# Performance work log

Hardware: AMD Instinct MI355X
Metric: run time of the kernel (lower is better)

## Reference

```python
import jax, jax.numpy as jnp
import numpy as np

B, N, T, D, H = 64, 207, 24, 128, 8
DK = D // H
EPS = 1e-5


def setup_inputs() -> dict:
    key = jax.random.key(0)
    ks = jax.random.split(key, 18)
    s = 1.0 / np.sqrt(D)
    inp = {
        "hidden": jax.random.normal(ks[0], (B, N, T, D), jnp.float32),
        "matrix": jax.random.uniform(ks[1], (B, T, N, N), jnp.float32) / N,
        "Wq": jax.random.normal(ks[2], (D, D), jnp.float32) * s,
        "bq": jnp.zeros((D,), jnp.float32),
        "Wk": jax.random.normal(ks[3], (D, D), jnp.float32) * s,
        "bk": jnp.zeros((D,), jnp.float32),
        "Wv": jax.random.normal(ks[4], (D, D), jnp.float32) * s,
        "bv": jnp.zeros((D,), jnp.float32),
        "Wo": jax.random.normal(ks[5], (D, D), jnp.float32) * s,
        "bo": jnp.zeros((D,), jnp.float32),
        "Wgcn": jax.random.normal(ks[6], (D, D), jnp.float32) * s,
        "bgcn": jnp.zeros((D,), jnp.float32),
        "Wgate": jax.random.normal(ks[7], (D, 2 * D), jnp.float32) * (1.0 / np.sqrt(2 * D)),
        "bgate": jnp.zeros((D,), jnp.float32),
        "gamma": jnp.ones((D,), jnp.float32),
        "beta": jnp.zeros((D,), jnp.float32),
    }
    return inp


def reference(hidden, matrix, Wq, bq, Wk, bk, Wv, bv, Wo, bo,
              Wgcn, bgcn, Wgate, bgate, gamma, beta):
    # ---- GCN branch: per-timestep A·X then channel mixing (dmodel->dmodel)
    # hidden: [B,N,T,D], matrix: [B,T,N,N] -> aggregated [B,N,T,D]
    agg = jnp.einsum('bntc,btnm->bmtc', hidden, matrix)
    gcn_out = agg @ Wgcn.T + bgcn                       # [B,N,T,D]

    # ---- Causal multi-head temporal attention
    q = (hidden @ Wq.T + bq).reshape(B, N, T, H, DK)
    k = (hidden @ Wk.T + bk).reshape(B, N, T, H, DK)
    v = (hidden @ Wv.T + bv).reshape(B, N, T, H, DK)
    scale = 1.0 / np.sqrt(DK)
    scores = jnp.einsum('bnthe,bnshe->bnhts', q, k)     # [B,N,H,T,T]
    causal = jnp.triu(jnp.ones((T, T), bool), k=1)      # mask future
    scores = jnp.where(causal, -jnp.inf, scores)
    attn = jax.nn.softmax(scale * scores, axis=-1)
    ctx = jnp.einsum('bnhts,bnshd->bnthd', attn, v).reshape(B, N, T, D)
    attn_out = ctx @ Wo.T + bo                          # [B,N,T,D]

    # ---- Gated fusion: concat -> linear -> batchnorm (training stats) -> sigmoid
    gate_in = jnp.concatenate([gcn_out, attn_out], axis=-1)  # [B,N,T,2D]
    g = gate_in @ Wgate.T + bgate                            # [B,N,T,D]
    mean = jnp.mean(g, axis=(0, 1, 2))
    var = jnp.var(g, axis=(0, 1, 2))
    g = (g - mean) * jax.lax.rsqrt(var + EPS) * gamma + beta
    z = jax.nn.sigmoid(g)
    return z * gcn_out + (1.0 - z) * attn_out
```

## Files before the change

kernel.cpp:

```cpp
#include <hip/hip_runtime.h>

#define B_ 64
#define N_ 207
#define T_ 24
#define D_ 128
#define H_ 8
#define MROWS (B_*N_*T_)
#define SELEMS ((size_t)MROWS * D_)
#define NBLK_FB 768
#define BNROWS_FB 414
#define NBLK_FUSED (MROWS/128)
#define EPS_ 1e-5f

typedef __attribute__((ext_vector_type(8))) short s16x8;
typedef __attribute__((ext_vector_type(4))) float f32x4;

#define MFMA16(a,b,c) __builtin_amdgcn_mfma_f32_16x16x32_bf16(a,b,c,0,0,0)

__device__ __forceinline__ float bfu2f(unsigned short u) {
  return __uint_as_float(((unsigned int)u) << 16);
}
__device__ __forceinline__ unsigned short f2bfu(float f) {
  unsigned int x = __float_as_uint(f);
  return (unsigned short)((x + 0x7fffu + ((x >> 16) & 1u)) >> 16);
}
__device__ __forceinline__ unsigned int packbf2(float lo, float hi) {
  return (unsigned int)f2bfu(lo) | ((unsigned int)f2bfu(hi) << 16);
}

__device__ __forceinline__ s16x8 fragA_from_f32(const float* __restrict__ p) {
  const float4 a = *(const float4*)p;
  const float4 b = *(const float4*)(p + 4);
  s16x8 r;
  r[0] = (short)f2bfu(a.x); r[1] = (short)f2bfu(a.y);
  r[2] = (short)f2bfu(a.z); r[3] = (short)f2bfu(a.w);
  r[4] = (short)f2bfu(b.x); r[5] = (short)f2bfu(b.y);
  r[6] = (short)f2bfu(b.z); r[7] = (short)f2bfu(b.w);
  return r;
}

__device__ __forceinline__ void epi_store_bf16(
    const f32x4 acc[2][8], const float* __restrict__ bias,
    unsigned short* __restrict__ Obase, unsigned short* __restrict__ lb, int l)
{
  const int lr = l & 15, lg = l >> 4;
  #pragma unroll
  for (int nt = 0; nt < 8; nt++) {
    const float b = bias[nt*16 + lr];
    #pragma unroll
    for (int mt = 0; mt < 2; mt++)
      #pragma unroll
      for (int r = 0; r < 4; r++)
        lb[(mt*16 + lg*4 + r)*136 + nt*16 + lr] = f2bfu(acc[mt][nt][r] + b);
  }
  #pragma unroll
  for (int p = 0; p < 8; p++) {
    const int c = p*64 + l;
    const int row = c >> 4, c8 = (c & 15) * 8;
    const s16x8 v = *(const s16x8*)&lb[row*136 + c8];
    *(s16x8*)(Obase + (size_t)row*D_ + c8) = v;
  }
}

__global__ __launch_bounds__(256) void k_wcast(
    const float* __restrict__ Wq, const float* __restrict__ Wk,
    const float* __restrict__ Wv, const float* __restrict__ Wo,
    const float* __restrict__ Wgcn, const float* __restrict__ Wgate,
    unsigned short* __restrict__ out)
{
  const int idx4 = (blockIdx.x * 256 + threadIdx.x) * 4;
  if (idx4 >= 114688) return;
  const float* src; int off;
  if      (idx4 < 16384) { src = Wq;    off = idx4; }
  else if (idx4 < 32768) { src = Wk;    off = idx4 - 16384; }
  else if (idx4 < 49152) { src = Wv;    off = idx4 - 32768; }
  else if (idx4 < 65536) { src = Wo;    off = idx4 - 49152; }
  else if (idx4 < 81920) { src = Wgcn;  off = idx4 - 65536; }
  else                   { src = Wgate; off = idx4 - 81920; }
  const float4 v = *(const float4*)(src + off);
  ushort4 u;
  u.x = f2bfu(v.x); u.y = f2bfu(v.y); u.z = f2bfu(v.z); u.w = f2bfu(v.w);
  *(ushort4*)(out + idx4) = u;
}

__global__ __launch_bounds__(256) void k_gcn2(
    const float* __restrict__ hidden, const float* __restrict__ matrix,
    const unsigned short* __restrict__ Wgcnb, const float* __restrict__ bgcn,
    unsigned short* __restrict__ gcn)
{
  __shared__ __align__(16) unsigned char smem[34816];
  unsigned short* Ms16 = (unsigned short*)smem;
  unsigned int*   Ms32 = (unsigned int*)smem;
  unsigned short* Hs16 = (unsigned short*)(smem + 10240);
  unsigned int*   Hs32 = (unsigned int*)(smem + 10240);
  unsigned short* GsAll = (unsigned short*)smem;

  const int tid = threadIdx.x;
  const int w = tid >> 6, l = tid & 63;
  const int lr = l & 15, lg = l >> 4;
  const int m0 = blockIdx.x * 128;
  const int by = (int)blockIdx.y;
  const int b = by / T_, t = by % T_;

  const int nn = (tid & 15) * 2;
  const int cb = (tid >> 4) * 8;

  const float* mbase = matrix + (size_t)(b*T_ + t)*N_*N_;
  const float* hbase = hidden + (size_t)b*N_*T_*D_ + (size_t)t*D_;

  f32x4 acc1[2][8];
  #pragma unroll
  for (int mt = 0; mt < 2; mt++)
    #pragma unroll
    for (int nt = 0; nt < 8; nt++)
      #pragma unroll
      for (int e = 0; e < 4; e++) acc1[mt][nt][e] = 0.f;

  for (int ch = 0; ch < 7; ++ch) {
    const int n0 = ch * 32;
    const int n_r0 = n0 + nn, n_r1 = n_r0 + 1;
    const bool rv0 = (n_r0 < N_), rv1 = (n_r1 < N_);
    const size_t nc0 = (size_t)(rv0 ? n_r0 : 0);
    const size_t nc1 = (size_t)(rv1 ? n_r1 : 0);

    float va[8], vb[8];
    {
      const float* r0 = mbase + nc0*N_ + m0 + cb;
      const float* r1 = mbase + nc1*N_ + m0 + cb;
      #pragma unroll
      for (int j = 0; j < 2; ++j) {
        const int mg = m0 + cb + j*4;
        if (mg + 3 < N_) {
          const float4 x0 = *(const float4*)(r0 + j*4);
          const float4 x1 = *(const float4*)(r1 + j*4);
          va[j*4+0]=x0.x; va[j*4+1]=x0.y; va[j*4+2]=x0.z; va[j*4+3]=x0.w;
          vb[j*4+0]=x1.x; vb[j*4+1]=x1.y; vb[j*4+2]=x1.z; vb[j*4+3]=x1.w;
        } else {
          #pragma unroll
          for (int e = 0; e < 4; ++e) {
            const bool ok = (mg + e) < N_;
            va[j*4+e] = ok ? r0[j*4+e] : 0.f;
            vb[j*4+e] = ok ? r1[j*4+e] : 0.f;
          }
        }
      }
      #pragma unroll
      for (int e = 0; e < 8; ++e) {
        if (!rv0) va[e] = 0.f;
        if (!rv1) vb[e] = 0.f;
      }
    }
    float ha[8], hb[8];
    {
      const float* r0 = hbase + nc0*(T_*D_) + cb;
      const float* r1 = hbase + nc1*(T_*D_) + cb;
      const float4 x0a = *(const float4*)(r0);
      const float4 x0b = *(const float4*)(r0 + 4);
      const float4 x1a = *(const float4*)(r1);
      const float4 x1b = *(const float4*)(r1 + 4);
      ha[0]=x0a.x; ha[1]=x0a.y; ha[2]=x0a.z; ha[3]=x0a.w;
      ha[4]=x0b.x; ha[5]=x0b.y; ha[6]=x0b.z; ha[7]=x0b.w;
      hb[0]=x1a.x; hb[1]=x1a.y; hb[2]=x1a.z; hb[3]=x1a.w;
      hb[4]=x1b.x; hb[5]=x1b.y; hb[6]=x1b.z; hb[7]=x1b.w;
      #pragma unroll
      for (int e = 0; e < 8; ++e) {
        if (!rv0) ha[e] = 0.f;
        if (!rv1) hb[e] = 0.f;
      }
    }
    __syncthreads();
    #pragma unroll
    for (int e = 0; e < 8; ++e)
      Ms32[(cb + e)*20 + (tid & 15)] = packbf2(va[e], vb[e]);
    #pragma unroll
    for (int e = 0; e < 8; ++e)
      Hs32[(cb + e)*20 + (tid & 15)] = packbf2(ha[e], hb[e]);
    __syncthreads();
    s16x8 af0 = *(const s16x8*)(Ms16 + (size_t)(w*32 +  0 + lr)*40 + lg*8);
    s16x8 af1 = *(const s16x8*)(Ms16 + (size_t)(w*32 + 16 + lr)*40 + lg*8);
    #pragma unroll
    for (int nt = 0; nt < 8; ++nt) {
      const s16x8 bf = *(const s16x8*)(Hs16 + (size_t)(nt*16 + lr)*40 + lg*8);
      acc1[0][nt] = MFMA16(af0, bf, acc1[0][nt]);
      acc1[1][nt] = MFMA16(af1, bf, acc1[1][nt]);
    }
  }

  __syncthreads();
  unsigned short* gs = GsAll + (size_t)w * (32*136);
  #pragma unroll
  for (int nt = 0; nt < 8; nt++)
    #pragma unroll
    for (int mt = 0; mt < 2; mt++)
      #pragma unroll
      for (int r = 0; r < 4; r++)
        gs[(mt*16 + lg*4 + r)*136 + nt*16 + lr] = f2bfu(acc1[mt][nt][r]);

  f32x4 acc2[2][8];
  #pragma unroll
  for (int mt = 0; mt < 2; mt++)
    #pragma unroll
    for (int nt = 0; nt < 8; nt++)
      #pragma unroll
      for (int e = 0; e < 4; e++) acc2[mt][nt][e] = 0.f;

  #pragma unroll
  for (int ks = 0; ks < 4; ++ks) {
    const s16x8 a0 = *(const s16x8*)(gs + (size_t)( 0 + lr)*136 + ks*32 + lg*8);
    const s16x8 a1 = *(const s16x8*)(gs + (size_t)(16 + lr)*136 + ks*32 + lg*8);
    #pragma unroll
    for (int nt = 0; nt < 8; ++nt) {
      const s16x8 bf = *(const s16x8*)(Wgcnb + (size_t)(nt*16 + lr)*D_ + ks*32 + lg*8);
      acc2[0][nt] = MFMA16(a0, bf, acc2[0][nt]);
      acc2[1][nt] = MFMA16(a1, bf, acc2[1][nt]);
    }
  }

  #pragma unroll
  for (int nt = 0; nt < 8; nt++) {
    const float bsc = bgcn[nt*16 + lr];
    #pragma unroll
    for (int mt = 0; mt < 2; mt++)
      #pragma unroll
      for (int r = 0; r < 4; r++)
        gs[(mt*16 + lg*4 + r)*136 + nt*16 + lr] = f2bfu(acc2[mt][nt][r] + bsc);
  }
  const size_t Obase = ((size_t)b*N_ + (m0 + w*32))*(size_t)(T_*D_) + (size_t)t*D_;
  #pragma unroll
  for (int p = 0; p < 8; p++) {
    const int c = p*64 + l;
    const int row = c >> 4, c8 = (c & 15) * 8;
    const int gm = m0 + w*32 + row;
    if (gm < N_) {
      const s16x8 v = *(const s16x8*)(gs + row*136 + c8);
      *(s16x8*)(gcn + Obase + (size_t)row*(T_*D_) + c8) = v;
    }
  }
}

__global__ __launch_bounds__(256) void k_qkv(
    const float* __restrict__ hidden,
    const unsigned short* __restrict__ Wqb, const unsigned short* __restrict__ Wkb,
    const unsigned short* __restrict__ Wvb,
    const float* __restrict__ bq, const float* __restrict__ bk,
    const float* __restrict__ bv,
    unsigned short* __restrict__ Q, unsigned short* __restrict__ K,
    unsigned short* __restrict__ V)
{
  __shared__ __align__(16) unsigned short lbuf[4][32*136];
  const int tid = threadIdx.x;
  const int w = tid >> 6, l = tid & 63;
  const int lr = l & 15, lg = l >> 4;
  const size_t m0 = (size_t)blockIdx.x * 128 + w * 32;

  s16x8 afr[2][4];
  #pragma unroll
  for (int mt = 0; mt < 2; mt++)
    #pragma unroll
    for (int ks = 0; ks < 4; ks++)
      afr[mt][ks] = fragA_from_f32(hidden + (m0 + mt*16 + lr)*D_ + ks*32 + lg*8);

  const unsigned short* Ws[3] = {Wqb, Wkb, Wvb};
  const float*          bs[3] = {bq, bk, bv};
  unsigned short*       Os[3] = {Q, K, V};
  #pragma unroll
  for (int out = 0; out < 3; out++) {
    const unsigned short* W = Ws[out];
    f32x4 acc[2][8];
    #pragma unroll
    for (int mt = 0; mt < 2; mt++)
      #pragma unroll
      for (int nt = 0; nt < 8; nt++)
        #pragma unroll
        for (int e = 0; e < 4; e++) acc[mt][nt][e] = 0.f;
    #pragma unroll
    for (int ks = 0; ks < 4; ks++) {
      #pragma unroll
      for (int nt = 0; nt < 8; nt++) {
        const s16x8 bf = *(const s16x8*)(W + (size_t)(nt*16 + lr)*D_ + ks*32 + lg*8);
        acc[0][nt] = MFMA16(afr[0][ks], bf, acc[0][nt]);
        acc[1][nt] = MFMA16(afr[1][ks], bf, acc[1][nt]);
      }
    }
    epi_store_bf16(acc, bs[out], Os[out] + m0*D_, lbuf[w], l);
  }
}

__global__ __launch_bounds__(256) void k_projWo(
    const unsigned short* __restrict__ A0,
    const unsigned short* __restrict__ Wb, const float* __restrict__ bias,
    unsigned short* __restrict__ OutP)
{
  __shared__ __align__(16) unsigned short lbuf[4][32*136];
  const int tid = threadIdx.x;
  const int w = tid >> 6, l = tid & 63;
  const int lr = l & 15, lg = l >> 4;
  const size_t m0 = (size_t)blockIdx.x * 128 + w * 32;

  f32x4 acc[2][8];
  #pragma unroll
  for (int mt = 0; mt < 2; mt++)
    #pragma unroll
    for (int nt = 0; nt < 8; nt++)
      #pragma unroll
      for (int e = 0; e < 4; e++) acc[mt][nt][e] = 0.f;

  #pragma unroll
  for (int ks = 0; ks < 4; ks++) {
    const s16x8 a0 = *(const s16x8*)(A0 + (m0 +  0 + lr)*D_ + ks*32 + lg*8);
    const s16x8 a1 = *(const s16x8*)(A0 + (m0 + 16 + lr)*D_ + ks*32 + lg*8);
    #pragma unroll
    for (int nt = 0; nt < 8; nt++) {
      const s16x8 bf = *(const s16x8*)(Wb + (size_t)(nt*16 + lr)*D_ + ks*32 + lg*8);
      acc[0][nt] = MFMA16(a0, bf, acc[0][nt]);
      acc[1][nt] = MFMA16(a1, bf, acc[1][nt]);
    }
  }
  epi_store_bf16(acc, bias, OutP + m0*D_, lbuf[w], l);
}

template<bool STATS>
__global__ __launch_bounds__(256) void k_gate(
    const unsigned short* __restrict__ A0, const unsigned short* __restrict__ A1,
    const unsigned short* __restrict__ Wb, const float* __restrict__ bias,
    float* __restrict__ Out, float* __restrict__ psum, float* __restrict__ psq)
{
  __shared__ float lbs[4*128], lbq[4*128];
  const int tid = threadIdx.x;
  const int w = tid >> 6, l = tid & 63;
  const int lr = l & 15, lg = l >> 4;
  const size_t m0 = (size_t)blockIdx.x * 128 + w * 32;

  f32x4 acc[2][8];
  #pragma unroll
  for (int mt = 0; mt < 2; mt++)
    #pragma unroll
    for (int nt = 0; nt < 8; nt++)
      #pragma unroll
      for (int e = 0; e < 4; e++) acc[mt][nt][e] = 0.f;

  #pragma unroll
  for (int ks = 0; ks < 8; ks++) {
    const unsigned short* Asrc = (ks >= 4) ? A1 : A0;
    const int kk = (ks >= 4) ? ks - 4 : ks;
    const s16x8 a0 = *(const s16x8*)(Asrc + (m0 +  0 + lr)*D_ + kk*32 + lg*8);
    const s16x8 a1 = *(const s16x8*)(Asrc + (m0 + 16 + lr)*D_ + kk*32 + lg*8);
    #pragma unroll
    for (int nt = 0; nt < 8; nt++) {
      const s16x8 bf = *(const s16x8*)(Wb + (size_t)(nt*16 + lr)*256 + ks*32 + lg*8);
      acc[0][nt] = MFMA16(a0, bf, acc[0][nt]);
      acc[1][nt] = MFMA16(a1, bf, acc[1][nt]);
    }
  }

  #pragma unroll
  for (int nt = 0; nt < 8; nt++) {
    const float b = bias[nt*16 + lr];
    float s = 0.f, q = 0.f;
    #pragma unroll
    for (int mt = 0; mt < 2; mt++)
      #pragma unroll
      for (int r = 0; r < 4; r++) {
        const float v = acc[mt][nt][r] + b;
        Out[(m0 + mt*16 + lg*4 + r)*D_ + nt*16 + lr] = v;
        if (STATS) { s += v; q += v*v; }
      }
    if (STATS) {
      s += __shfl_xor(s, 16); s += __shfl_xor(s, 32);
      q += __shfl_xor(q, 16); q += __shfl_xor(q, 32);
      if (lg == 0) {
        lbs[w*128 + nt*16 + lr] = s;
        lbq[w*128 + nt*16 + lr] = q;
      }
    }
  }
  if (STATS) {
    __syncthreads();
    if (tid < 128) {
      const float ss = lbs[tid] + lbs[128 + tid] + lbs[256 + tid] + lbs[384 + tid];
      const float qq = lbq[tid] + lbq[128 + tid] + lbq[256 + tid] + lbq[384 + tid];
      psum[(size_t)blockIdx.x*128 + tid] = ss;
      psq [(size_t)blockIdx.x*128 + tid] = qq;
    }
  }
}

__global__ __launch_bounds__(192) void k_attn2(
    const unsigned short* __restrict__ Q, const unsigned short* __restrict__ K,
    const unsigned short* __restrict__ V, unsigned short* __restrict__ CTX)
{
  __shared__ __align__(16) unsigned short Qs[T_*D_], Ks[T_*D_], Vs[T_*D_];
  const int tid = threadIdx.x;
  const size_t base = (size_t)blockIdx.x * (T_*D_);
  for (int i = tid; i < (T_*D_)/8; i += 192) {
    ((int4*)Qs)[i] = ((const int4*)(Q + base))[i];
    ((int4*)Ks)[i] = ((const int4*)(K + base))[i];
    ((int4*)Vs)[i] = ((const int4*)(V + base))[i];
  }
  __syncthreads();

  const int h = tid / T_, t = tid % T_;
  const int hb = h * 16;
  float q[16];
  #pragma unroll
  for (int e = 0; e < 16; e++) q[e] = bfu2f(Qs[t*D_ + hb + e]);

  float p[T_];
  float mx = -1e30f;
  #pragma unroll
  for (int s = 0; s < T_; s++) {
    float d = 0.f;
    #pragma unroll
    for (int e = 0; e < 16; e++) d += q[e] * bfu2f(Ks[s*D_ + hb + e]);
    d *= 0.25f;
    d = (s <= t) ? d : -1e30f;
    p[s] = d;
    mx = fmaxf(mx, d);
  }
  float den = 0.f;
  #pragma unroll
  for (int s = 0; s < T_; s++) {
    float e = __expf(p[s] - mx);
    e = (s <= t) ? e : 0.f;
    p[s] = e;
    den += e;
  }
  const float rd = 1.f / den;
  float o[16];
  #pragma unroll
  for (int e = 0; e < 16; e++) o[e] = 0.f;
  #pragma unroll
  for (int s = 0; s < T_; s++) {
    const float ps = p[s];
    #pragma unroll
    for (int e = 0; e < 16; e++) o[e] += ps * bfu2f(Vs[s*D_ + hb + e]);
  }
  s16x8 r0, r1;
  #pragma unroll
  for (int e = 0; e < 8; e++) { r0[e] = (short)f2bfu(o[e]*rd); r1[e] = (short)f2bfu(o[8+e]*rd); }
  *(s16x8*)(CTX + base + (size_t)t*D_ + hb)     = r0;
  *(s16x8*)(CTX + base + (size_t)t*D_ + hb + 8) = r1;
}

__global__ __launch_bounds__(256) void k_bnstats(
    const float* __restrict__ g, float* __restrict__ psum, float* __restrict__ psq)
{
  const int tid = threadIdx.x;
  const int c4 = (tid & 31) * 4, sub = tid >> 5;
  const size_t r0 = (size_t)blockIdx.x * BNROWS_FB;
  float4 s = make_float4(0.f,0.f,0.f,0.f), q = make_float4(0.f,0.f,0.f,0.f);
  for (int i = sub; i < BNROWS_FB; i += 8) {
    const float4 x = *(const float4*)(g + (r0 + i)*D_ + c4);
    s.x += x.x; s.y += x.y; s.z += x.z; s.w += x.w;
    q.x += x.x*x.x; q.y += x.y*x.y; q.z += x.z*x.z; q.w += x.w*x.w;
  }
  __shared__ float ls[8*128], lq[8*128];
  *(float4*)&ls[sub*128 + c4] = s;
  *(float4*)&lq[sub*128 + c4] = q;
  __syncthreads();
  if (tid < 128) {
    float ss = 0.f, qq = 0.f;
    #pragma unroll
    for (int k = 0; k < 8; k++) { ss += ls[k*128 + tid]; qq += lq[k*128 + tid]; }
    psum[(size_t)blockIdx.x*128 + tid] = ss;
    psq [(size_t)blockIdx.x*128 + tid] = qq;
  }
}

__global__ __launch_bounds__(1024) void k_bnfinal(
    const float* __restrict__ psum, const float* __restrict__ psq, int nblk,
    float* __restrict__ meanv, float* __restrict__ invstdv)
{
  const int tid = threadIdx.x;
  const int sub = tid >> 7, ch = tid & 127;
  float s = 0.f, q = 0.f;
  for (int i = sub; i < nblk; i += 8) {
    s += psum[(size_t)i*128 + ch];
    q += psq [(size_t)i*128 + ch];
  }
  __shared__ float ls[8*128], lq[8*128];
  ls[sub*128 + ch] = s; lq[sub*128 + ch] = q;
  __syncthreads();
  if (tid < 128) {
    float ss = 0.f, qq = 0.f;
    #pragma unroll
    for (int k = 0; k < 8; k++) { ss += ls[k*128 + tid]; qq += lq[k*128 + tid]; }
    const float mean = ss / (float)MROWS;
    const float var  = qq / (float)MROWS - mean*mean;
    meanv[tid] = mean;
    invstdv[tid] = rsqrtf(var + EPS_);
  }
}

__global__ __launch_bounds__(256) void k_final(
    float* __restrict__ g,
    const unsigned short* __restrict__ gcn, const unsigned short* __restrict__ attn,
    const float* __restrict__ meanv, const float* __restrict__ invstdv,
    const float* __restrict__ gamma, const float* __restrict__ beta)
{
  const size_t tot4 = SELEMS >> 2;
  for (size_t i4 = (size_t)blockIdx.x*blockDim.x + threadIdx.x; i4 < tot4;
       i4 += (size_t)gridDim.x*blockDim.x) {
    const int c4 = (int)(i4 & 31) * 4;
    const float4 gv = ((const float4*)g)[i4];
    const ushort4 gc = ((const ushort4*)gcn)[i4];
    const ushort4 at = ((const ushort4*)attn)[i4];
    const float4 m4 = *(const float4*)(meanv + c4);
    const float4 s4 = *(const float4*)(invstdv + c4);
    const float4 ga = *(const float4*)(gamma + c4);
    const float4 be = *(const float4*)(beta + c4);
    float4 outv;
    { const float y = (gv.x - m4.x)*s4.x*ga.x + be.x;
      const float z = 1.f/(1.f + __expf(-y));
      outv.x = z*bfu2f(gc.x) + (1.f - z)*bfu2f(at.x); }
    { const float y = (gv.y - m4.y)*s4.y*ga.y + be.y;
      const float z = 1.f/(1.f + __expf(-y));
      outv.y = z*bfu2f(gc.y) + (1.f - z)*bfu2f(at.y); }
    { const float y = (gv.z - m4.z)*s4.z*ga.z + be.z;
      const float z = 1.f/(1.f + __expf(-y));
      outv.z = z*bfu2f(gc.z) + (1.f - z)*bfu2f(at.z); }
    { const float y = (gv.w - m4.w)*s4.w*ga.w + be.w;
      const float z = 1.f/(1.f + __expf(-y));
      outv.w = z*bfu2f(gc.w) + (1.f - z)*bfu2f(at.w); }
    ((float4*)g)[i4] = outv;
  }
}

extern "C" void kernel_launch(void* const* d_in, const int* in_sizes, int n_in,
                              void* d_out, int out_size, void* d_ws, size_t ws_size,
                              hipStream_t stream)
{
  (void)in_sizes; (void)n_in; (void)out_size;
  const float* hidden = (const float*)d_in[0];
  const float* matrix = (const float*)d_in[1];
  const float* Wq   = (const float*)d_in[2];  const float* bq    = (const float*)d_in[3];
  const float* Wk   = (const float*)d_in[4];  const float* bk    = (const float*)d_in[5];
  const float* Wv   = (const float*)d_in[6];  const float* bv    = (const float*)d_in[7];
  const float* Wo   = (const float*)d_in[8];  const float* bo    = (const float*)d_in[9];
  const float* Wgcn = (const float*)d_in[10]; const float* bgcn  = (const float*)d_in[11];
  const float* Wgate= (const float*)d_in[12]; const float* bgate = (const float*)d_in[13];
  const float* gamma= (const float*)d_in[14]; const float* beta  = (const float*)d_in[15];
  float* out = (float*)d_out;

  unsigned short* WB = (unsigned short*)d_ws;
  unsigned short* Wqb    = WB;
  unsigned short* Wkb    = WB + 16384;
  unsigned short* Wvb    = WB + 32768;
  unsigned short* Wob    = WB + 49152;
  unsigned short* Wgcnb  = WB + 65536;
  unsigned short* Wgateb = WB + 81920;
  unsigned short* X1     = WB + 114688;
  unsigned short* X2     = X1 + SELEMS;
  float* psum    = (float*)(X2 + SELEMS);

  const size_t base_bytes = (size_t)(WB + 114688 - (unsigned short*)d_ws)*2
                          + 2*SELEMS*2;
  const size_t fused_bytes = base_bytes + ((size_t)NBLK_FUSED*128*2 + 256)*4;
  const bool fused = (ws_size >= fused_bytes);
  const int nblk = fused ? NBLK_FUSED : NBLK_FB;
  float* psq     = psum + (size_t)nblk*128;
  float* meanv   = psq  + (size_t)nblk*128;
  float* invstdv = meanv + 128;

  unsigned short* D1 = (unsigned short*)d_out;
  unsigned short* D2 = D1 + SELEMS;

  k_wcast<<<112, 256, 0, stream>>>(Wq, Wk, Wv, Wo, Wgcn, Wgate, WB);
  k_gcn2 <<<dim3(2, B_*T_), 256, 0, stream>>>(hidden, matrix, Wgcnb, bgcn, X2);
  k_qkv  <<<MROWS/128, 256, 0, stream>>>(hidden, Wqb, Wkb, Wvb, bq, bk, bv,
                                         D1, D2, X1);
  k_attn2<<<B_*N_, 192, 0, stream>>>(D1, D2, X1, D1);
  k_projWo<<<MROWS/128, 256, 0, stream>>>(D1, Wob, bo, X1);
  if (fused) {
    k_gate<true><<<MROWS/128, 256, 0, stream>>>(X2, X1, Wgateb, bgate, out, psum, psq);
  } else {
    k_gate<false><<<MROWS/128, 256, 0, stream>>>(X2, X1, Wgateb, bgate, out, psum, psq);
    k_bnstats<<<NBLK_FB, 256, 0, stream>>>(out, psum, psq);
  }
  k_bnfinal<<<1, 1024, 0, stream>>>(psum, psq, nblk, meanv, invstdv);
  k_final<<<2048, 256, 0, stream>>>(out, X2, X1, meanv, invstdv, gamma, beta);
}
```

Before: 857.4 us.

## Fuse QKV projection, causal attention and Wo projection into one kernel; double-buffer GCN loads

Replaces the separate QKV-projection, attention and output-projection kernels with one kernel per (batch,node) that converts hidden to bf16 in shared memory, computes Q/K/V with MFMA, runs causal softmax attention, and applies Wo. Q, K, V and the context never go to global memory. The GCN kernel also double-buffers its LDS tiles and prefetches the next chunk into registers, which removes one barrier per iteration. In exchange, each fused block has only 24 valid rows padded to 32, so MFMA work is partly wasted, and the bigger LDS footprint may lower occupancy.

```diff
diff --git a/kernel.cpp b/kernel.cpp
--- a/kernel.cpp
+++ b/kernel.cpp
@@ -26,40 +26,6 @@
 }
 __device__ __forceinline__ unsigned int packbf2(float lo, float hi) {
   return (unsigned int)f2bfu(lo) | ((unsigned int)f2bfu(hi) << 16);
-}
-
-__device__ __forceinline__ s16x8 fragA_from_f32(const float* __restrict__ p) {
-  const float4 a = *(const float4*)p;
-  const float4 b = *(const float4*)(p + 4);
-  s16x8 r;
-  r[0] = (short)f2bfu(a.x); r[1] = (short)f2bfu(a.y);
-  r[2] = (short)f2bfu(a.z); r[3] = (short)f2bfu(a.w);
-  r[4] = (short)f2bfu(b.x); r[5] = (short)f2bfu(b.y);
-  r[6] = (short)f2bfu(b.z); r[7] = (short)f2bfu(b.w);
-  return r;
-}
-
-__device__ __forceinline__ void epi_store_bf16(
-    const f32x4 acc[2][8], const float* __restrict__ bias,
-    unsigned short* __restrict__ Obase, unsigned short* __restrict__ lb, int l)
-{
-  const int lr = l & 15, lg = l >> 4;
-  #pragma unroll
-  for (int nt = 0; nt < 8; nt++) {
-    const float b = bias[nt*16 + lr];
-    #pragma unroll
-    for (int mt = 0; mt < 2; mt++)
-      #pragma unroll
-      for (int r = 0; r < 4; r++)
-        lb[(mt*16 + lg*4 + r)*136 + nt*16 + lr] = f2bfu(acc[mt][nt][r] + b);
-  }
-  #pragma unroll
-  for (int p = 0; p < 8; p++) {
-    const int c = p*64 + l;
-    const int row = c >> 4, c8 = (c & 15) * 8;
-    const s16x8 v = *(const s16x8*)&lb[row*136 + c8];
-    *(s16x8*)(Obase + (size_t)row*D_ + c8) = v;
-  }
 }
 
 __global__ __launch_bounds__(256) void k_wcast(
@@ -83,16 +49,66 @@
   *(ushort4*)(out + idx4) = u;
 }
 
+__device__ __forceinline__ void gcn_load(
+    const float* __restrict__ mbase, const float* __restrict__ hbase,
+    int m0, int nn, int cb, int ch,
+    float va[8], float vb[8], float ha[8], float hb[8])
+{
+  const int n_r0 = ch*32 + nn, n_r1 = n_r0 + 1;
+  const bool rv0 = (n_r0 < N_), rv1 = (n_r1 < N_);
+  const size_t nc0 = (size_t)(rv0 ? n_r0 : 0);
+  const size_t nc1 = (size_t)(rv1 ? n_r1 : 0);
+  {
+    const float* r0 = mbase + nc0*N_ + m0 + cb;
+    const float* r1 = mbase + nc1*N_ + m0 + cb;
+    #pragma unroll
+    for (int j = 0; j < 2; ++j) {
+      const int mg = m0 + cb + j*4;
+      if (mg + 3 < N_) {
+        const float4 x0 = *(const float4*)(r0 + j*4);
+        const float4 x1 = *(const float4*)(r1 + j*4);
+        va[j*4+0]=x0.x; va[j*4+1]=x0.y; va[j*4+2]=x0.z; va[j*4+3]=x0.w;
+        vb[j*4+0]=x1.x; vb[j*4+1]=x1.y; vb[j*4+2]=x1.z; vb[j*4+3]=x1.w;
+      } else {
+        #pragma unroll
+        for (int e = 0; e < 4; ++e) {
+          const bool ok = (mg + e) < N_;
+          va[j*4+e] = ok ? r0[j*4+e] : 0.f;
+          vb[j*4+e] = ok ? r1[j*4+e] : 0.f;
+        }
+      }
+    }
+    #pragma unroll
+    for (int e = 0; e < 8; ++e) {
+      if (!rv0) va[e] = 0.f;
+      if (!rv1) vb[e] = 0.f;
+    }
+  }
+  {
+    const float* r0 = hbase + nc0*(T_*D_) + cb;
+    const float* r1 = hbase + nc1*(T_*D_) + cb;
+    const float4 x0a = *(const float4*)(r0);
+    const float4 x0b = *(const float4*)(r0 + 4);
+    const float4 x1a = *(const float4*)(r1);
+    const float4 x1b = *(const float4*)(r1 + 4);
+    ha[0]=x0a.x; ha[1]=x0a.y; ha[2]=x0a.z; ha[3]=x0a.w;
+    ha[4]=x0b.x; ha[5]=x0b.y; ha[6]=x0b.z; ha[7]=x0b.w;
+    hb[0]=x1a.x; hb[1]=x1a.y; hb[2]=x1a.z; hb[3]=x1a.w;
+    hb[4]=x1b.x; hb[5]=x1b.y; hb[6]=x1b.z; hb[7]=x1b.w;
+    #pragma unroll
+    for (int e = 0; e < 8; ++e) {
+      if (!rv0) ha[e] = 0.f;
+      if (!rv1) hb[e] = 0.f;
+    }
+  }
+}
+
 __global__ __launch_bounds__(256) void k_gcn2(
     const float* __restrict__ hidden, const float* __restrict__ matrix,
     const unsigned short* __restrict__ Wgcnb, const float* __restrict__ bgcn,
     unsigned short* __restrict__ gcn)
 {
-  __shared__ __align__(16) unsigned char smem[34816];
-  unsigned short* Ms16 = (unsigned short*)smem;
-  unsigned int*   Ms32 = (unsigned int*)smem;
-  unsigned short* Hs16 = (unsigned short*)(smem + 10240);
-  unsigned int*   Hs32 = (unsigned int*)(smem + 10240);
+  __shared__ __align__(16) unsigned char smem[40960];
   unsigned short* GsAll = (unsigned short*)smem;
 
   const int tid = threadIdx.x;
@@ -116,71 +132,30 @@
       #pragma unroll
       for (int e = 0; e < 4; e++) acc1[mt][nt][e] = 0.f;
 
+  float va[8], vb[8], ha[8], hb[8];
+  gcn_load(mbase, hbase, m0, nn, cb, 0, va, vb, ha, hb);
+
+  #pragma unroll
   for (int ch = 0; ch < 7; ++ch) {
-    const int n0 = ch * 32;
-    const int n_r0 = n0 + nn, n_r1 = n_r0 + 1;
-    const bool rv0 = (n_r0 < N_), rv1 = (n_r1 < N_);
-    const size_t nc0 = (size_t)(rv0 ? n_r0 : 0);
-    const size_t nc1 = (size_t)(rv1 ? n_r1 : 0);
-
-    float va[8], vb[8];
-    {
-      const float* r0 = mbase + nc0*N_ + m0 + cb;
-      const float* r1 = mbase + nc1*N_ + m0 + cb;
-      #pragma unroll
-      for (int j = 0; j < 2; ++j) {
-        const int mg = m0 + cb + j*4;
-        if (mg + 3 < N_) {
-          const float4 x0 = *(const float4*)(r0 + j*4);
-          const float4 x1 = *(const float4*)(r1 + j*4);
-          va[j*4+0]=x0.x; va[j*4+1]=x0.y; va[j*4+2]=x0.z; va[j*4+3]=x0.w;
-          vb[j*4+0]=x1.x; vb[j*4+1]=x1.y; vb[j*4+2]=x1.z; vb[j*4+3]=x1.w;
-        } else {
-          #pragma unroll
-          for (int e = 0; e < 4; ++e) {
-            const bool ok = (mg + e) < N_;
-            va[j*4+e] = ok ? r0[j*4+e] : 0.f;
-            vb[j*4+e] = ok ? r1[j*4+e] : 0.f;
-          }
-        }
-      }
-      #pragma unroll
-      for (int e = 0; e < 8; ++e) {
-        if (!rv0) va[e] = 0.f;
-        if (!rv1) vb[e] = 0.f;
-      }
-    }
-    float ha[8], hb[8];
-    {
-      const float* r0 = hbase + nc0*(T_*D_) + cb;
-      const float* r1 = hbase + nc1*(T_*D_) + cb;
-      const float4 x0a = *(const float4*)(r0);
-      const float4 x0b = *(const float4*)(r0 + 4);
-      const float4 x1a = *(const float4*)(r1);
-      const float4 x1b = *(const float4*)(r1 + 4);
-      ha[0]=x0a.x; ha[1]=x0a.y; ha[2]=x0a.z; ha[3]=x0a.w;
-      ha[4]=x0b.x; ha[5]=x0b.y; ha[6]=x0b.z; ha[7]=x0b.w;
-      hb[0]=x1a.x; hb[1]=x1a.y; hb[2]=x1a.z; hb[3]=x1a.w;
-      hb[4]=x1b.x; hb[5]=x1b.y; hb[6]=x1b.z; hb[7]=x1b.w;
-      #pragma unroll
-      for (int e = 0; e < 8; ++e) {
-        if (!rv0) ha[e] = 0.f;
-        if (!rv1) hb[e] = 0.f;
-      }
-    }
+    unsigned char* base = smem + ((ch & 1) ? 20480 : 0);
+    unsigned int* M32 = (unsigned int*)base;
+    unsigned int* H32 = (unsigned int*)(base + 10240);
+    #pragma unroll
+    for (int e = 0; e < 8; ++e)
+      M32[(cb + e)*20 + (tid & 15)] = packbf2(va[e], vb[e]);
+    #pragma unroll
+    for (int e = 0; e < 8; ++e)
+      H32[(cb + e)*20 + (tid & 15)] = packbf2(ha[e], hb[e]);
+    if (ch < 6)
+      gcn_load(mbase, hbase, m0, nn, cb, ch + 1, va, vb, ha, hb);
     __syncthreads();
-    #pragma unroll
-    for (int e = 0; e < 8; ++e)
-      Ms32[(cb + e)*20 + (tid & 15)] = packbf2(va[e], vb[e]);
-    #pragma unroll
-    for (int e = 0; e < 8; ++e)
-      Hs32[(cb + e)*20 + (tid & 15)] = packbf2(ha[e], hb[e]);
-    __syncthreads();
-    s16x8 af0 = *(const s16x8*)(Ms16 + (size_t)(w*32 +  0 + lr)*40 + lg*8);
-    s16x8 af1 = *(const s16x8*)(Ms16 + (size_t)(w*32 + 16 + lr)*40 + lg*8);
+    const unsigned short* M16 = (const unsigned short*)M32;
+    const unsigned short* H16 = (const unsigned short*)H32;
+    const s16x8 af0 = *(const s16x8*)(M16 + (size_t)(w*32 +  0 + lr)*40 + lg*8);
+    const s16x8 af1 = *(const s16x8*)(M16 + (size_t)(w*32 + 16 + lr)*40 + lg*8);
     #pragma unroll
     for (int nt = 0; nt < 8; ++nt) {
-      const s16x8 bf = *(const s16x8*)(Hs16 + (size_t)(nt*16 + lr)*40 + lg*8);
+      const s16x8 bf = *(const s16x8*)(H16 + (size_t)(nt*16 + lr)*40 + lg*8);
       acc1[0][nt] = MFMA16(af0, bf, acc1[0][nt]);
       acc1[1][nt] = MFMA16(af1, bf, acc1[1][nt]);
     }
@@ -238,85 +213,183 @@
   }
 }
 
-__global__ __launch_bounds__(256) void k_qkv(
+__global__ __launch_bounds__(256) void k_attn3(
     const float* __restrict__ hidden,
     const unsigned short* __restrict__ Wqb, const unsigned short* __restrict__ Wkb,
-    const unsigned short* __restrict__ Wvb,
+    const unsigned short* __restrict__ Wvb, const unsigned short* __restrict__ Wob,
     const float* __restrict__ bq, const float* __restrict__ bk,
-    const float* __restrict__ bv,
-    unsigned short* __restrict__ Q, unsigned short* __restrict__ K,
-    unsigned short* __restrict__ V)
-{
-  __shared__ __align__(16) unsigned short lbuf[4][32*136];
+    const float* __restrict__ bv, const float* __restrict__ bo,
+    unsigned short* __restrict__ attnO)
+{
+  __shared__ __align__(16) unsigned short Xs[32*136], Qs[32*136],
+                                          Ks[32*136], Vs[32*136];
   const int tid = threadIdx.x;
   const int w = tid >> 6, l = tid & 63;
   const int lr = l & 15, lg = l >> 4;
-  const size_t m0 = (size_t)blockIdx.x * 128 + w * 32;
-
-  s16x8 afr[2][4];
+  const size_t bn = blockIdx.x;
+  const float* X = hidden + bn * (size_t)(T_*D_);
+
+  for (int i = tid; i < 32*16; i += 256) {
+    const int row = i >> 4, g8 = (i & 15) * 8;
+    s16x8 v;
+    if (row < T_) {
+      const float4 a  = *(const float4*)(X + (size_t)row*D_ + g8);
+      const float4 b2 = *(const float4*)(X + (size_t)row*D_ + g8 + 4);
+      v[0]=(short)f2bfu(a.x);  v[1]=(short)f2bfu(a.y);
+      v[2]=(short)f2bfu(a.z);  v[3]=(short)f2bfu(a.w);
+      v[4]=(short)f2bfu(b2.x); v[5]=(short)f2bfu(b2.y);
+      v[6]=(short)f2bfu(b2.z); v[7]=(short)f2bfu(b2.w);
+    } else {
+      #pragma unroll
+      for (int e = 0; e < 8; e++) v[e] = 0;
+    }
+    *(s16x8*)&Xs[row*136 + g8] = v;
+  }
+  __syncthreads();
+
+  s16x8 af[2][4];
   #pragma unroll
   for (int mt = 0; mt < 2; mt++)
     #pragma unroll
     for (int ks = 0; ks < 4; ks++)
-      afr[mt][ks] = fragA_from_f32(hidden + (m0 + mt*16 + lr)*D_ + ks*32 + lg*8);
-
-  const unsigned short* Ws[3] = {Wqb, Wkb, Wvb};
-  const float*          bs[3] = {bq, bk, bv};
-  unsigned short*       Os[3] = {Q, K, V};
-  #pragma unroll
-  for (int out = 0; out < 3; out++) {
-    const unsigned short* W = Ws[out];
-    f32x4 acc[2][8];
+      af[mt][ks] = *(const s16x8*)&Xs[(mt*16 + lr)*136 + ks*32 + lg*8];
+
+  const unsigned short* Wp[3] = {Wqb, Wkb, Wvb};
+  const float*          bp[3] = {bq, bk, bv};
+  unsigned short*       Op[3] = {Qs, Ks, Vs};
+  #pragma unroll
+  for (int o = 0; o < 3; o++) {
+    f32x4 acc[2][2];
     #pragma unroll
     for (int mt = 0; mt < 2; mt++)
       #pragma unroll
-      for (int nt = 0; nt < 8; nt++)
+      for (int nt = 0; nt < 2; nt++)
         #pragma unroll
         for (int e = 0; e < 4; e++) acc[mt][nt][e] = 0.f;
     #pragma unroll
     for (int ks = 0; ks < 4; ks++) {
       #pragma unroll
-      for (int nt = 0; nt < 8; nt++) {
-        const s16x8 bf = *(const s16x8*)(W + (size_t)(nt*16 + lr)*D_ + ks*32 + lg*8);
-        acc[0][nt] = MFMA16(afr[0][ks], bf, acc[0][nt]);
-        acc[1][nt] = MFMA16(afr[1][ks], bf, acc[1][nt]);
-      }
-    }
-    epi_store_bf16(acc, bs[out], Os[out] + m0*D_, lbuf[w], l);
-  }
-}
-
-__global__ __launch_bounds__(256) void k_projWo(
-    const unsigned short* __restrict__ A0,
-    const unsigned short* __restrict__ Wb, const float* __restrict__ bias,
-    unsigned short* __restrict__ OutP)
-{
-  __shared__ __align__(16) unsigned short lbuf[4][32*136];
-  const int tid = threadIdx.x;
-  const int w = tid >> 6, l = tid & 63;
-  const int lr = l & 15, lg = l >> 4;
-  const size_t m0 = (size_t)blockIdx.x * 128 + w * 32;
-
-  f32x4 acc[2][8];
+      for (int nt = 0; nt < 2; nt++) {
+        const s16x8 bf = *(const s16x8*)(Wp[o] + (size_t)(w*32 + nt*16 + lr)*D_ + ks*32 + lg*8);
+        acc[0][nt] = MFMA16(af[0][ks], bf, acc[0][nt]);
+        acc[1][nt] = MFMA16(af[1][ks], bf, acc[1][nt]);
+      }
+    }
+    #pragma unroll
+    for (int nt = 0; nt < 2; nt++) {
+      const float bb = bp[o][w*32 + nt*16 + lr];
+      #pragma unroll
+      for (int mt = 0; mt < 2; mt++)
+        #pragma unroll
+        for (int r = 0; r < 4; r++)
+          Op[o][(mt*16 + lg*4 + r)*136 + w*32 + nt*16 + lr] =
+              f2bfu(acc[mt][nt][r] + bb);
+    }
+  }
+  __syncthreads();
+
+  if (tid < H_*T_) {
+    const int h = tid / T_, t = tid % T_;
+    const int hb = h * 16;
+    float q[16];
+    {
+      const s16x8 q0 = *(const s16x8*)&Qs[t*136 + hb];
+      const s16x8 q1 = *(const s16x8*)&Qs[t*136 + hb + 8];
+      #pragma unroll
+      for (int e = 0; e < 8; e++) {
+        q[e]   = bfu2f((unsigned short)q0[e]);
+        q[8+e] = bfu2f((unsigned short)q1[e]);
+      }
+    }
+    float p[T_];
+    float mx = -1e30f;
+    #pragma unroll
+    for (int s = 0; s < T_; s++) {
+      const s16x8 k0 = *(const s16x8*)&Ks[s*136 + hb];
+      const s16x8 k1 = *(const s16x8*)&Ks[s*136 + hb + 8];
+      float d = 0.f;
+      #pragma unroll
+      for (int e = 0; e < 8; e++) {
+        d += q[e]   * bfu2f((unsigned short)k0[e]);
+        d += q[8+e] * bfu2f((unsigned short)k1[e]);
+      }
+      d *= 0.25f;
+      d = (s <= t) ? d : -1e30f;
+      p[s] = d;
+      mx = fmaxf(mx, d);
+    }
+    float den = 0.f;
+    #pragma unroll
+    for (int s = 0; s < T_; s++) {
+      float e = __expf(p[s] - mx);
+      e = (s <= t) ? e : 0.f;
+      p[s] = e;
+      den += e;
+    }
+    const float rd = 1.f / den;
+    float o[16];
+    #pragma unroll
+    for (int e = 0; e < 16; e++) o[e] = 0.f;
+    #pragma unroll
+    for (int s = 0; s < T_; s++) {
+      const float ps = p[s];
+      const s16x8 v0 = *(const s16x8*)&Vs[s*136 + hb];
+      const s16x8 v1 = *(const s16x8*)&Vs[s*136 + hb + 8];
+      #pragma unroll
+      for (int e = 0; e < 8; e++) {
+        o[e]   += ps * bfu2f((unsigned short)v0[e]);
+        o[8+e] += ps * bfu2f((unsigned short)v1[e]);
+      }
+    }
+    s16x8 r0, r1;
+    #pragma unroll
+    for (int e = 0; e < 8; e++) {
+      r0[e] = (short)f2bfu(o[e]   * rd);
+      r1[e] = (short)f2bfu(o[8+e] * rd);
+    }
+    *(s16x8*)&Qs[t*136 + hb]     = r0;
+    *(s16x8*)&Qs[t*136 + hb + 8] = r1;
+  }
+  __syncthreads();
+
+  s16x8 cf[2][4];
   #pragma unroll
   for (int mt = 0; mt < 2; mt++)
     #pragma unroll
-    for (int nt = 0; nt < 8; nt++)
-      #pragma unroll
-      for (int e = 0; e < 4; e++) acc[mt][nt][e] = 0.f;
-
+    for (int ks = 0; ks < 4; ks++)
+      cf[mt][ks] = *(const s16x8*)&Qs[(mt*16 + lr)*136 + ks*32 + lg*8];
+  f32x4 acc2[2][2];
+  #pragma unroll
+  for (int mt = 0; mt < 2; mt++)
+    #pragma unroll
+    for (int nt = 0; nt < 2; nt++)
+      #pragma unroll
+      for (int e = 0; e < 4; e++) acc2[mt][nt][e] = 0.f;
   #pragma unroll
   for (int ks = 0; ks < 4; ks++) {
-    const s16x8 a0 = *(const s16x8*)(A0 + (m0 +  0 + lr)*D_ + ks*32 + lg*8);
-    const s16x8 a1 = *(const s16x8*)(A0 + (m0 + 16 + lr)*D_ + ks*32 + lg*8);
-    #pragma unroll
-    for (int nt = 0; nt < 8; nt++) {
-      const s16x8 bf = *(const s16x8*)(Wb + (size_t)(nt*16 + lr)*D_ + ks*32 + lg*8);
-      acc[0][nt] = MFMA16(a0, bf, acc[0][nt]);
-      acc[1][nt] = MFMA16(a1, bf, acc[1][nt]);
-    }
-  }
-  epi_store_bf16(acc, bias, OutP + m0*D_, lbuf[w], l);
+    #pragma unroll
+    for (int nt = 0; nt < 2; nt++) {
+      const s16x8 bf = *(const s16x8*)(Wob + (size_t)(w*32 + nt*16 + lr)*D_ + ks*32 + lg*8);
+      acc2[0][nt] = MFMA16(cf[0][ks], bf, acc2[0][nt]);
+      acc2[1][nt] = MFMA16(cf[1][ks], bf, acc2[1][nt]);
+    }
+  }
+  #pragma unroll
+  for (int nt = 0; nt < 2; nt++) {
+    const float bb = bo[w*32 + nt*16 + lr];
+    #pragma unroll
+    for (int mt = 0; mt < 2; mt++)
+      #pragma unroll
+      for (int r = 0; r < 4; r++)
+        Xs[(mt*16 + lg*4 + r)*136 + w*32 + nt*16 + lr] =
+            f2bfu(acc2[mt][nt][r] + bb);
+  }
+  __syncthreads();
+  unsigned short* O = attnO + bn * (size_t)(T_*D_);
+  for (int i = tid; i < 24*16; i += 256) {
+    const int row = i >> 4, g8 = (i & 15) * 8;
+    *(s16x8*)(O + (size_t)row*D_ + g8) = *(const s16x8*)&Xs[row*136 + g8];
+  }
 }
 
 template<bool STATS>
@@ -383,63 +456,6 @@
       psq [(size_t)blockIdx.x*128 + tid] = qq;
     }
   }
-}
-
-__global__ __launch_bounds__(192) void k_attn2(
-    const unsigned short* __restrict__ Q, const unsigned short* __restrict__ K,
-    const unsigned short* __restrict__ V, unsigned short* __restrict__ CTX)
-{
-  __shared__ __align__(16) unsigned short Qs[T_*D_], Ks[T_*D_], Vs[T_*D_];
-  const int tid = threadIdx.x;
-  const size_t base = (size_t)blockIdx.x * (T_*D_);
-  for (int i = tid; i < (T_*D_)/8; i += 192) {
-    ((int4*)Qs)[i] = ((const int4*)(Q + base))[i];
-    ((int4*)Ks)[i] = ((const int4*)(K + base))[i];
-    ((int4*)Vs)[i] = ((const int4*)(V + base))[i];
-  }
-  __syncthreads();
-
-  const int h = tid / T_, t = tid % T_;
-  const int hb = h * 16;
-  float q[16];
-  #pragma unroll
-  for (int e = 0; e < 16; e++) q[e] = bfu2f(Qs[t*D_ + hb + e]);
-
-  float p[T_];
-  float mx = -1e30f;
-  #pragma unroll
-  for (int s = 0; s < T_; s++) {
-    float d = 0.f;
-    #pragma unroll
-    for (int e = 0; e < 16; e++) d += q[e] * bfu2f(Ks[s*D_ + hb + e]);
-    d *= 0.25f;
-    d = (s <= t) ? d : -1e30f;
-    p[s] = d;
-    mx = fmaxf(mx, d);
-  }
-  float den = 0.f;
-  #pragma unroll
-  for (int s = 0; s < T_; s++) {
-    float e = __expf(p[s] - mx);
-    e = (s <= t) ? e : 0.f;
-    p[s] = e;
-    den += e;
-  }
-  const float rd = 1.f / den;
-  float o[16];
-  #pragma unroll
-  for (int e = 0; e < 16; e++) o[e] = 0.f;
-  #pragma unroll
-  for (int s = 0; s < T_; s++) {
-    const float ps = p[s];
-    #pragma unroll
-    for (int e = 0; e < 16; e++) o[e] += ps * bfu2f(Vs[s*D_ + hb + e]);
-  }
-  s16x8 r0, r1;
-  #pragma unroll
-  for (int e = 0; e < 8; e++) { r0[e] = (short)f2bfu(o[e]*rd); r1[e] = (short)f2bfu(o[8+e]*rd); }
-  *(s16x8*)(CTX + base + (size_t)t*D_ + hb)     = r0;
-  *(s16x8*)(CTX + base + (size_t)t*D_ + hb + 8) = r1;
 }
 
 __global__ __launch_bounds__(256) void k_bnstats(
@@ -562,15 +578,10 @@
   float* meanv   = psq  + (size_t)nblk*128;
   float* invstdv = meanv + 128;
 
-  unsigned short* D1 = (unsigned short*)d_out;
-  unsigned short* D2 = D1 + SELEMS;
-
   k_wcast<<<112, 256, 0, stream>>>(Wq, Wk, Wv, Wo, Wgcn, Wgate, WB);
   k_gcn2 <<<dim3(2, B_*T_), 256, 0, stream>>>(hidden, matrix, Wgcnb, bgcn, X2);
-  k_qkv  <<<MROWS/128, 256, 0, stream>>>(hidden, Wqb, Wkb, Wvb, bq, bk, bv,
-                                         D1, D2, X1);
-  k_attn2<<<B_*N_, 192, 0, stream>>>(D1, D2, X1, D1);
-  k_projWo<<<MROWS/128, 256, 0, stream>>>(D1, Wob, bo, X1);
+  k_attn3<<<B_*N_, 256, 0, stream>>>(hidden, Wqb, Wkb, Wvb, Wob,
+                                     bq, bk, bv, bo, X1);
   if (fused) {
     k_gate<true><<<MROWS/128, 256, 0, stream>>>(X2, X1, Wgateb, bgate, out, psum, psq);
   } else {
```

Result: faster. 815.6 us (-4.9%).
